# Kernel tuning notes

Measured on AMD Instinct MI355X. Metric: run time of the kernel, lower is better.

The kernel has to match this reference:

```python
import jax, jax.numpy as jnp
import numpy as np

EPS = 1e-12  # matches torch F.normalize eps


def _l2_normalize(x, axis=-1):
    # torch.F.normalize: x / max(||x||, eps)
    n = jnp.sqrt(jnp.sum(x * x, axis=axis, keepdims=True))
    return x / jnp.maximum(n, EPS)


def setup_inputs() -> dict:
    N, n_classes, embed_dim = 32768, 1000, 1024
    key = jax.random.key(0)
    k_feat, k_lab, k_proto = jax.random.split(key, 3)

    features = jax.random.normal(k_feat, (N, embed_dim), dtype=jnp.float32)

    # one-hot float labels, as expected by `torch.matmul(labels, self.mean_class)`
    y = jax.random.randint(k_lab, (N,), 0, n_classes)
    labels = jax.nn.one_hot(y, n_classes, dtype=jnp.float32)

    # predefined prototypes: orthonormal rows (ortho_group.rvs equivalent via QR)
    g = jax.random.normal(k_proto, (embed_dim, embed_dim), dtype=jnp.float32)
    q, _ = jnp.linalg.qr(g)
    mean_class = q[:n_classes]  # [n_classes, embed_dim], orthonormal rows

    return {"features": features, "labels": labels, "mean_class": mean_class}


def reference(features, labels, mean_class):
    # features: [N, D]; labels: [N, C] one-hot; mean_class: [C, D]
    # (3-D feature mean-pooling branch not exercised: inputs are 2-D)
    proto_y = labels @ mean_class                 # [N, D]
    f = _l2_normalize(features, axis=1)
    p = _l2_normalize(proto_y, axis=1)
    # diag(f @ p.T) == rowwise dot product -> same math, O(N*D) not O(N^2*D)
    cos = jnp.einsum("nd,nd->n", f, p)            # [N]
    return jnp.mean(1.0 - cos)
```

## Files before the change

### kernel.cpp

```cpp
#include <hip/hip_runtime.h>

constexpr int N_CLASSES = 1000;
constexpr int EMBED     = 1024;
constexpr int ROWS_PER_BLOCK = 8;

__global__ __launch_bounds__(256) void angular_rows_kernel(
    const float* __restrict__ features,
    const float* __restrict__ labels,
    const float* __restrict__ mean_class,
    float* __restrict__ partials,
    int n_rows)
{
    const int tid  = threadIdx.x;
    const int lane = tid & 63;
    const int wave = tid >> 6;

    __shared__ float s_a[4], s_b[4], s_c[4];
    __shared__ int   s_idx;

    float block_acc = 0.0f;

    for (int r = 0; r < ROWS_PER_BLOCK; ++r) {
        const int row = blockIdx.x * ROWS_PER_BLOCK + r;
        if (row >= n_rows) break;

        const float4 f = ((const float4*)(features + (size_t)row * EMBED))[tid];

        float idxf = 0.0f;
        if (tid < N_CLASSES / 4) {
            const float4 v = ((const float4*)(labels + (size_t)row * N_CLASSES))[tid];
            const float c = (float)(tid * 4);
            idxf = v.x * c + v.y * (c + 1.0f) + v.z * (c + 2.0f) + v.w * (c + 3.0f);
        }
        #pragma unroll
        for (int off = 32; off > 0; off >>= 1)
            idxf += __shfl_down(idxf, off, 64);
        if (lane == 0) s_a[wave] = idxf;
        __syncthreads();
        if (tid == 0) s_idx = (int)(s_a[0] + s_a[1] + s_a[2] + s_a[3] + 0.5f);
        __syncthreads();
        const int cls = s_idx;

        const float4 p = ((const float4*)(mean_class + (size_t)cls * EMBED))[tid];

        float ff = f.x*f.x + f.y*f.y + f.z*f.z + f.w*f.w;
        float pp = p.x*p.x + p.y*p.y + p.z*p.z + p.w*p.w;
        float fp = f.x*p.x + f.y*p.y + f.z*p.z + f.w*p.w;
        #pragma unroll
        for (int off = 32; off > 0; off >>= 1) {
            ff += __shfl_down(ff, off, 64);
            pp += __shfl_down(pp, off, 64);
            fp += __shfl_down(fp, off, 64);
        }
        if (lane == 0) { s_a[wave] = ff; s_b[wave] = pp; s_c[wave] = fp; }
        __syncthreads();
        if (tid == 0) {
            const float FF = s_a[0] + s_a[1] + s_a[2] + s_a[3];
            const float PP = s_b[0] + s_b[1] + s_b[2] + s_b[3];
            const float FP = s_c[0] + s_c[1] + s_c[2] + s_c[3];
            const float denom = fmaxf(sqrtf(FF), 1e-12f) * fmaxf(sqrtf(PP), 1e-12f);
            block_acc += 1.0f - FP / denom;
        }
        __syncthreads();
    }

    if (tid == 0) partials[blockIdx.x] = block_acc;
}

__global__ __launch_bounds__(256) void reduce_partials_kernel(
    const float* __restrict__ partials, int num_partials,
    float* __restrict__ out, float inv_n)
{
    const int tid  = threadIdx.x;
    const int lane = tid & 63;
    const int wave = tid >> 6;
    __shared__ float s_red[4];

    float acc = 0.0f;
    for (int i = tid; i < num_partials; i += 256)
        acc += partials[i];
    #pragma unroll
    for (int off = 32; off > 0; off >>= 1)
        acc += __shfl_down(acc, off, 64);
    if (lane == 0) s_red[wave] = acc;
    __syncthreads();
    if (tid == 0)
        out[0] = (s_red[0] + s_red[1] + s_red[2] + s_red[3]) * inv_n;
}

extern "C" void kernel_launch(void* const* d_in, const int* in_sizes, int n_in,
                              void* d_out, int out_size, void* d_ws, size_t ws_size,
                              hipStream_t stream) {
    const float* features   = (const float*)d_in[0];
    const float* labels     = (const float*)d_in[1];
    const float* mean_class = (const float*)d_in[2];
    float* out = (float*)d_out;
    float* partials = (float*)d_ws;

    const int n_rows = in_sizes[0] / EMBED;
    const int num_blocks = (n_rows + ROWS_PER_BLOCK - 1) / ROWS_PER_BLOCK;

    angular_rows_kernel<<<num_blocks, 256, 0, stream>>>(
        features, labels, mean_class, partials, n_rows);
    reduce_partials_kernel<<<1, 256, 0, stream>>>(
        partials, num_blocks, out, 1.0f / (float)n_rows);
}
```

Before: 289.3 us.

## Process one row per wavefront with grid-stride loop, removing block barriers

Each 64-lane wave now handles a whole row, loading four float4 chunks of features and labels per lane and reducing with xor shuffles, so the per-row __syncthreads and shared-memory round trips are gone. The grid is fixed at 1024 blocks and waves stride over rows, with a single block-level reduction at the end. This raises memory-level parallelism per lane and removes synchronization latency. The trade-off is more registers per lane and a fixed grid size that may not suit other row counts.

```diff
diff --git a/kernel.cpp b/kernel.cpp
--- a/kernel.cpp
+++ b/kernel.cpp
@@ -2,7 +2,6 @@
 
 constexpr int N_CLASSES = 1000;
 constexpr int EMBED     = 1024;
-constexpr int ROWS_PER_BLOCK = 8;
 
 __global__ __launch_bounds__(256) void angular_rows_kernel(
     const float* __restrict__ features,
@@ -15,56 +14,70 @@
     const int lane = tid & 63;
     const int wave = tid >> 6;
 
-    __shared__ float s_a[4], s_b[4], s_c[4];
-    __shared__ int   s_idx;
+    const int wave_id = (blockIdx.x * blockDim.x + tid) >> 6;
+    const int n_waves = (gridDim.x * blockDim.x) >> 6;
 
-    float block_acc = 0.0f;
+    float wave_acc = 0.0f;
 
-    for (int r = 0; r < ROWS_PER_BLOCK; ++r) {
-        const int row = blockIdx.x * ROWS_PER_BLOCK + r;
-        if (row >= n_rows) break;
+    for (int row = wave_id; row < n_rows; row += n_waves) {
+        const float4* frow = (const float4*)(features + (size_t)row * EMBED);
+        float4 f0 = frow[lane];
+        float4 f1 = frow[lane + 64];
+        float4 f2 = frow[lane + 128];
+        float4 f3 = frow[lane + 192];
 
-        const float4 f = ((const float4*)(features + (size_t)row * EMBED))[tid];
+        const float4* lrow = (const float4*)(labels + (size_t)row * N_CLASSES);
+        float4 l0 = lrow[lane];
+        float4 l1 = lrow[lane + 64];
+        float4 l2 = lrow[lane + 128];
+        float4 l3 = (lane < N_CLASSES / 4 - 192) ? lrow[lane + 192]
+                                                 : make_float4(0, 0, 0, 0);
 
         float idxf = 0.0f;
-        if (tid < N_CLASSES / 4) {
-            const float4 v = ((const float4*)(labels + (size_t)row * N_CLASSES))[tid];
-            const float c = (float)(tid * 4);
-            idxf = v.x * c + v.y * (c + 1.0f) + v.z * (c + 2.0f) + v.w * (c + 3.0f);
+        {
+            float c0 = (float)(lane * 4);
+            idxf += l0.x * c0 + l0.y * (c0 + 1.f) + l0.z * (c0 + 2.f) + l0.w * (c0 + 3.f);
+            float c1 = (float)((lane + 64) * 4);
+            idxf += l1.x * c1 + l1.y * (c1 + 1.f) + l1.z * (c1 + 2.f) + l1.w * (c1 + 3.f);
+            float c2 = (float)((lane + 128) * 4);
+            idxf += l2.x * c2 + l2.y * (c2 + 1.f) + l2.z * (c2 + 2.f) + l2.w * (c2 + 3.f);
+            float c3 = (float)((lane + 192) * 4);
+            idxf += l3.x * c3 + l3.y * (c3 + 1.f) + l3.z * (c3 + 2.f) + l3.w * (c3 + 3.f);
         }
         #pragma unroll
-        for (int off = 32; off > 0; off >>= 1)
-            idxf += __shfl_down(idxf, off, 64);
-        if (lane == 0) s_a[wave] = idxf;
-        __syncthreads();
-        if (tid == 0) s_idx = (int)(s_a[0] + s_a[1] + s_a[2] + s_a[3] + 0.5f);
-        __syncthreads();
-        const int cls = s_idx;
+        for (int m = 1; m < 64; m <<= 1)
+            idxf += __shfl_xor(idxf, m, 64);
+        const int cls = (int)(idxf + 0.5f);
 
-        const float4 p = ((const float4*)(mean_class + (size_t)cls * EMBED))[tid];
+        const float4* prow = (const float4*)(mean_class + (size_t)cls * EMBED);
+        float4 p0 = prow[lane];
+        float4 p1 = prow[lane + 64];
+        float4 p2 = prow[lane + 128];
+        float4 p3 = prow[lane + 192];
 
-        float ff = f.x*f.x + f.y*f.y + f.z*f.z + f.w*f.w;
-        float pp = p.x*p.x + p.y*p.y + p.z*p.z + p.w*p.w;
-        float fp = f.x*p.x + f.y*p.y + f.z*p.z + f.w*p.w;
+        float ff = 0.f, pp = 0.f, fp = 0.f;
+        #define DOT3(F, P) \
+            ff += F.x*F.x + F.y*F.y + F.z*F.z + F.w*F.w; \
+            pp += P.x*P.x + P.y*P.y + P.z*P.z + P.w*P.w; \
+            fp += F.x*P.x + F.y*P.y + F.z*P.z + F.w*P.w;
+        DOT3(f0, p0) DOT3(f1, p1) DOT3(f2, p2) DOT3(f3, p3)
+        #undef DOT3
+
         #pragma unroll
-        for (int off = 32; off > 0; off >>= 1) {
-            ff += __shfl_down(ff, off, 64);
-            pp += __shfl_down(pp, off, 64);
-            fp += __shfl_down(fp, off, 64);
+        for (int m = 1; m < 64; m <<= 1) {
+            ff += __shfl_xor(ff, m, 64);
+            pp += __shfl_xor(pp, m, 64);
+            fp += __shfl_xor(fp, m, 64);
         }
-        if (lane == 0) { s_a[wave] = ff; s_b[wave] = pp; s_c[wave] = fp; }
-        __syncthreads();
-        if (tid == 0) {
-            const float FF = s_a[0] + s_a[1] + s_a[2] + s_a[3];
-            const float PP = s_b[0] + s_b[1] + s_b[2] + s_b[3];
-            const float FP = s_c[0] + s_c[1] + s_c[2] + s_c[3];
-            const float denom = fmaxf(sqrtf(FF), 1e-12f) * fmaxf(sqrtf(PP), 1e-12f);
-            block_acc += 1.0f - FP / denom;
-        }
-        __syncthreads();
+        const float denom = fmaxf(sqrtf(ff), 1e-12f) * fmaxf(sqrtf(pp), 1e-12f);
+        wave_acc += 1.0f - fp / denom;
     }
 
-    if (tid == 0) partials[blockIdx.x] = block_acc;
+    __shared__ float s_red[4];
+    if (lane == 0) s_red[wave] = wave_acc;
+    __syncthreads();
+    if (tid == 0)
+        partials[blockIdx.x] = s_red[0] + s_red[1] + s_red[2] + s_red[3];
 }
 
 __global__ __launch_bounds__(256) void reduce_partials_kernel(
@@ -80,8 +93,8 @@
     for (int i = tid; i < num_partials; i += 256)
         acc += partials[i];
     #pragma unroll
-    for (int off = 32; off > 0; off >>= 1)
-        acc += __shfl_down(acc, off, 64);
+    for (int m = 1; m < 64; m <<= 1)
+        acc += __shfl_xor(acc, m, 64);
     if (lane == 0) s_red[wave] = acc;
     __syncthreads();
     if (tid == 0)
@@ -98,7 +111,7 @@
     float* partials = (float*)d_ws;
 
     const int n_rows = in_sizes[0] / EMBED;
-    const int num_blocks = (n_rows + ROWS_PER_BLOCK - 1) / ROWS_PER_BLOCK;
+    const int num_blocks = 1024;
 
     angular_rows_kernel<<<num_blocks, 256, 0, stream>>>(
         features, labels, mean_class, partials, n_rows);
```

New measurement: 278.2 us. 3.8% less time.
